# Performance work log

Hardware: AMD Instinct MI355X
Metric: run time of the kernel (lower is better)

Reference implementation:

```python
import jax, jax.numpy as jnp
import numpy as np

PROP_TIME = 8  # matches init kwarg prop_time


def setup_inputs() -> dict:
    key = jax.random.key(0)
    k1, k2, k3, k4, k5 = jax.random.split(key, 5)
    B, H, W = 8, 480, 640
    return {
        "guided1": jax.random.normal(k1, (B, 9, H, W), dtype=jnp.float32),
        "guided2": jax.random.normal(k2, (B, 9, H, W), dtype=jnp.float32),
        "guided3": jax.random.normal(k3, (B, 9, H, W), dtype=jnp.float32),
        "fuse": jax.random.uniform(k4, (B, 3, H, W), dtype=jnp.float32),
        "x": jax.random.normal(k5, (B, 1, H, W), dtype=jnp.float32),
    }


def _neighbors(x, d):
    """Gather the 3x3 dilated neighborhood of a [B,1,H,W] map -> [B,9,H,W].
    Equivalent to F.unfold(x, 3, dilation=d, padding=d) reshaped to spatial."""
    B, _, H, W = x.shape
    xp = jnp.pad(x[:, 0], ((0, 0), (d, d), (d, d)))  # B, H+2d, W+2d
    return jnp.stack(
        [xp[:, i * d:i * d + H, j * d:j * d + W] for i in range(3) for j in range(3)],
        axis=1,
    )


def reference(guided1, guided2, guided3, fuse, x):
    # per-pixel affinity kernels, normalized over the 9 taps
    k1 = jax.nn.softmax(guided1, axis=1)
    k2 = jax.nn.softmax(guided2, axis=1)
    k3 = jax.nn.softmax(guided3, axis=1)
    f1, f2, f3 = fuse[:, 0:1], fuse[:, 1:2], fuse[:, 2:3]
    for _ in range(PROP_TIME):
        o1 = jnp.sum(_neighbors(x, 1) * k1, axis=1, keepdims=True)  # B,1,H,W
        o2 = jnp.sum(_neighbors(x, 2) * k2, axis=1, keepdims=True)
        o3 = jnp.sum(_neighbors(x, 3) * k3, axis=1, keepdims=True)
        x = o1 * f1 + o2 * f2 + o3 * f3
    return x
```

## Files before the change

### kernel.cpp

```cpp
#include <hip/hip_runtime.h>

typedef __attribute__((ext_vector_type(4))) float    float4v;
typedef __attribute__((ext_vector_type(8))) _Float16 half8v;
typedef __attribute__((ext_vector_type(4))) _Float16 half4v;

constexpr int B_ = 8;
constexpr int H_ = 480;
constexpr int W_ = 640;
constexpr int HW = H_ * W_;
constexpr int N  = B_ * HW;
constexpr int WPP = 28;

__global__ __launch_bounds__(256) void wprep_kernel(
    const float* __restrict__ g1, const float* __restrict__ g2,
    const float* __restrict__ g3, const float* __restrict__ fuse,
    _Float16* __restrict__ w)
{
    const int p  = blockIdx.x * 256 + threadIdx.x;
    const int b  = p / HW;
    const int hw = p - b * HW;

    _Float16 wl[WPP];
    wl[27] = (_Float16)0.f;

    const float* gs[3] = {g1, g2, g3};
#pragma unroll
    for (int d = 0; d < 3; ++d) {
        const float* gb = gs[d] + (size_t)b * 9 * HW + hw;
        float e[9];
        float m = -1e30f;
#pragma unroll
        for (int c = 0; c < 9; ++c) {
            e[c] = gb[(size_t)c * HW];
            m = fmaxf(m, e[c]);
        }
        float s = 0.f;
#pragma unroll
        for (int c = 0; c < 9; ++c) {
            e[c] = __expf(e[c] - m);
            s += e[c];
        }
        const float f = fuse[((size_t)b * 3 + d) * HW + hw] / s;
#pragma unroll
        for (int c = 0; c < 9; ++c)
            wl[d * 9 + c] = (_Float16)(e[c] * f);
    }

    _Float16* wp = w + (size_t)p * WPP;
    *(half8v*)(wp + 0)  = *(half8v*)(wl + 0);
    *(half8v*)(wp + 8)  = *(half8v*)(wl + 8);
    *(half8v*)(wp + 16) = *(half8v*)(wl + 16);
    *(half4v*)(wp + 24) = *(half4v*)(wl + 24);
}

__global__ __launch_bounds__(256) void prop_kernel(
    const float* __restrict__ xin, const _Float16* __restrict__ w,
    float* __restrict__ xout)
{
    const int j  = blockIdx.x * 64 + (threadIdx.x & 63);
    const int i  = blockIdx.y * 4  + (threadIdx.x >> 6);
    const int b  = blockIdx.z;
    const int hw = i * W_ + j;
    const int p  = b * HW + hw;

    const _Float16* wp = w + (size_t)p * WPP;
    const half8v w0 = *(const half8v*)(wp + 0);
    const half8v w1 = *(const half8v*)(wp + 8);
    const half8v w2 = *(const half8v*)(wp + 16);
    const half4v w3 = *(const half4v*)(wp + 24);

    _Float16 wl[27];
#pragma unroll
    for (int k = 0; k < 8; ++k) { wl[k] = w0[k]; wl[8 + k] = w1[k]; wl[16 + k] = w2[k]; }
#pragma unroll
    for (int k = 0; k < 3; ++k) wl[24 + k] = w3[k];

    const float* xb = xin + (size_t)b * HW;
    float acc = 0.f;
#pragma unroll
    for (int d = 1; d <= 3; ++d) {
#pragma unroll
        for (int ki = 0; ki < 3; ++ki) {
            const int ii = i + (ki - 1) * d;
            const bool vi = (unsigned)ii < (unsigned)H_;
#pragma unroll
            for (int kj = 0; kj < 3; ++kj) {
                const int jj = j + (kj - 1) * d;
                float xv = 0.f;
                if (vi && (unsigned)jj < (unsigned)W_)
                    xv = xb[ii * W_ + jj];
                acc = fmaf(xv, (float)wl[(d - 1) * 9 + ki * 3 + kj], acc);
            }
        }
    }
    xout[p] = acc;
}

extern "C" void kernel_launch(void* const* d_in, const int* in_sizes, int n_in,
                              void* d_out, int out_size, void* d_ws, size_t ws_size,
                              hipStream_t stream)
{
    const float* g1   = (const float*)d_in[0];
    const float* g2   = (const float*)d_in[1];
    const float* g3   = (const float*)d_in[2];
    const float* fuse = (const float*)d_in[3];
    const float* x    = (const float*)d_in[4];
    float* out = (float*)d_out;

    char* ws = (char*)d_ws;
    _Float16* w = (_Float16*)ws;
    float* xa = (float*)(ws + (size_t)N * WPP * 2);
    float* xb = xa + N;

    wprep_kernel<<<N / 256, 256, 0, stream>>>(g1, g2, g3, fuse, w);

    const dim3 pgrid(W_ / 64, H_ / 4, B_);
    const float* src = x;
    float* bufs[2] = {xa, xb};
    for (int t = 0; t < 8; ++t) {
        float* dst = (t == 7) ? out : bufs[t & 1];
        prop_kernel<<<pgrid, 256, 0, stream>>>(src, w, dst);
        src = dst;
    }
}
```

Baseline: 301.8 us.

## Fuse two propagation steps per launch with shared-memory halo tiles

Replaces the per-step propagation kernel with one that does two propagation iterations per launch. Each block stages a 52x80 input tile with a 6-pixel halo in LDS. It computes the intermediate step over a 46x72 region, holding the fp16 weights for 4 pixels per thread in registers, then writes that result back to LDS and computes the final 40x64 outputs. This halves the number of launches and global passes over the weight and x buffers. The cost is recomputing the halo, roughly 29% extra work on the first step, plus a large 832-thread block with higher register pressure.

New measurement: 366.4 us. 21.4% more time.

```diff
diff --git a/kernel.cpp b/kernel.cpp
--- a/kernel.cpp
+++ b/kernel.cpp
@@ -11,6 +11,15 @@
 constexpr int N  = B_ * HW;
 constexpr int WPP = 28;
 
+constexpr int TI = 40;
+constexpr int TJ = 64;
+constexpr int LR = 52;
+constexpr int LC = 80;
+constexpr int QROWS = 46;
+constexpr int QCOLS = 18;
+constexpr int NOWN  = QROWS * QCOLS;
+constexpr int BLK   = 832;
+
 __global__ __launch_bounds__(256) void wprep_kernel(
     const float* __restrict__ g1, const float* __restrict__ g2,
     const float* __restrict__ g3, const float* __restrict__ fuse,
@@ -53,47 +62,136 @@
     *(half4v*)(wp + 24) = *(half4v*)(wl + 24);
 }
 
-__global__ __launch_bounds__(256) void prop_kernel(
+__device__ __forceinline__ float wsel(const half8v& a, const half8v& b,
+                                      const half8v& c, const half4v& d, int t)
+{
+    if (t < 8)  return (float)a[t];
+    if (t < 16) return (float)b[t - 8];
+    if (t < 24) return (float)c[t - 16];
+    return (float)d[t - 24];
+}
+
+__global__ __launch_bounds__(BLK) void prop2_kernel(
     const float* __restrict__ xin, const _Float16* __restrict__ w,
     float* __restrict__ xout)
 {
-    const int j  = blockIdx.x * 64 + (threadIdx.x & 63);
-    const int i  = blockIdx.y * 4  + (threadIdx.x >> 6);
-    const int b  = blockIdx.z;
-    const int hw = i * W_ + j;
-    const int p  = b * HW + hw;
-
-    const _Float16* wp = w + (size_t)p * WPP;
-    const half8v w0 = *(const half8v*)(wp + 0);
-    const half8v w1 = *(const half8v*)(wp + 8);
-    const half8v w2 = *(const half8v*)(wp + 16);
-    const half4v w3 = *(const half4v*)(wp + 24);
-
-    _Float16 wl[27];
-#pragma unroll
-    for (int k = 0; k < 8; ++k) { wl[k] = w0[k]; wl[8 + k] = w1[k]; wl[16 + k] = w2[k]; }
-#pragma unroll
-    for (int k = 0; k < 3; ++k) wl[24 + k] = w3[k];
-
+    __shared__ float xs[LR * LC];
+
+    const int tid   = threadIdx.x;
+    const int tileJ = blockIdx.x;
+    const int tileI = blockIdx.y;
+    const int b     = blockIdx.z;
+    const int ti0   = tileI * TI;
+    const int tj0   = tileJ * TJ;
     const float* xb = xin + (size_t)b * HW;
-    float acc = 0.f;
-#pragma unroll
-    for (int d = 1; d <= 3; ++d) {
-#pragma unroll
-        for (int ki = 0; ki < 3; ++ki) {
-            const int ii = i + (ki - 1) * d;
-            const bool vi = (unsigned)ii < (unsigned)H_;
-#pragma unroll
-            for (int kj = 0; kj < 3; ++kj) {
-                const int jj = j + (kj - 1) * d;
-                float xv = 0.f;
-                if (vi && (unsigned)jj < (unsigned)W_)
-                    xv = xb[ii * W_ + jj];
-                acc = fmaf(xv, (float)wl[(d - 1) * 9 + ki * 3 + kj], acc);
-            }
-        }
-    }
-    xout[p] = acc;
+
+    for (int idx = tid; idx < LR * LC / 4; idx += BLK) {
+        const int r   = idx / (LC / 4);
+        const int q   = idx % (LC / 4);
+        const int gi  = ti0 + r - 6;
+        const int gj0 = tj0 + q * 4 - 8;
+        float4v v = {0.f, 0.f, 0.f, 0.f};
+        if ((unsigned)gi < (unsigned)H_) {
+            if (gj0 >= 0 && gj0 + 3 < W_) {
+                v = *(const float4v*)(xb + (size_t)gi * W_ + gj0);
+            } else {
+#pragma unroll
+                for (int k = 0; k < 4; ++k) {
+                    const int gj = gj0 + k;
+                    if ((unsigned)gj < (unsigned)W_) v[k] = xb[(size_t)gi * W_ + gj];
+                }
+            }
+        }
+        *(float4v*)&xs[r * LC + q * 4] = v;
+    }
+
+    const bool owner = (tid < NOWN);
+    const int qr  = tid / QCOLS;
+    const int qc  = tid % QCOLS;
+    const int li  = 3 + qr;
+    const int lj0 = 4 + qc * 4;
+    const int gi  = ti0 + qr - 3;
+    const int gj0 = tj0 + qc * 4 - 4;
+
+    const half8v z8 = {0, 0, 0, 0, 0, 0, 0, 0};
+    const half4v z4 = {0, 0, 0, 0};
+    half8v w0[4] = {z8, z8, z8, z8};
+    half8v w1[4] = {z8, z8, z8, z8};
+    half8v w2[4] = {z8, z8, z8, z8};
+    half4v w3[4] = {z4, z4, z4, z4};
+
+    if (owner && (unsigned)gi < (unsigned)H_) {
+#pragma unroll
+        for (int k = 0; k < 4; ++k) {
+            const int gj = gj0 + k;
+            if ((unsigned)gj < (unsigned)W_) {
+                const _Float16* wp = w + ((size_t)b * HW + (size_t)gi * W_ + gj) * WPP;
+                w0[k] = *(const half8v*)(wp + 0);
+                w1[k] = *(const half8v*)(wp + 8);
+                w2[k] = *(const half8v*)(wp + 16);
+                w3[k] = *(const half4v*)(wp + 24);
+            }
+        }
+    }
+    __syncthreads();
+
+    float x1[4] = {0.f, 0.f, 0.f, 0.f};
+    if (owner) {
+#pragma unroll
+        for (int dd = 0; dd < 3; ++dd) {
+            const int d = dd + 1;
+#pragma unroll
+            for (int ki = 0; ki < 3; ++ki) {
+                const int base = (li + (ki - 1) * d) * LC + lj0;
+                float win[12];
+                *(float4v*)&win[0] = *(const float4v*)&xs[base - 4];
+                *(float4v*)&win[4] = *(const float4v*)&xs[base];
+                *(float4v*)&win[8] = *(const float4v*)&xs[base + 4];
+#pragma unroll
+                for (int kj = 0; kj < 3; ++kj) {
+                    const int t   = dd * 9 + ki * 3 + kj;
+                    const int off = (kj - 1) * d + 4;
+#pragma unroll
+                    for (int k = 0; k < 4; ++k)
+                        x1[k] = fmaf(win[off + k], wsel(w0[k], w1[k], w2[k], w3[k], t), x1[k]);
+                }
+            }
+        }
+    }
+    __syncthreads();
+
+    if (owner) {
+        float4v v; v[0] = x1[0]; v[1] = x1[1]; v[2] = x1[2]; v[3] = x1[3];
+        *(float4v*)&xs[li * LC + lj0] = v;
+    }
+    __syncthreads();
+
+    const bool outq = owner && (qr >= 3) && (qr < 3 + TI) && (qc >= 1) && (qc < 17);
+    if (outq) {
+        float x2[4] = {0.f, 0.f, 0.f, 0.f};
+#pragma unroll
+        for (int dd = 0; dd < 3; ++dd) {
+            const int d = dd + 1;
+#pragma unroll
+            for (int ki = 0; ki < 3; ++ki) {
+                const int base = (li + (ki - 1) * d) * LC + lj0;
+                float win[12];
+                *(float4v*)&win[0] = *(const float4v*)&xs[base - 4];
+                *(float4v*)&win[4] = *(const float4v*)&xs[base];
+                *(float4v*)&win[8] = *(const float4v*)&xs[base + 4];
+#pragma unroll
+                for (int kj = 0; kj < 3; ++kj) {
+                    const int t   = dd * 9 + ki * 3 + kj;
+                    const int off = (kj - 1) * d + 4;
+#pragma unroll
+                    for (int k = 0; k < 4; ++k)
+                        x2[k] = fmaf(win[off + k], wsel(w0[k], w1[k], w2[k], w3[k], t), x2[k]);
+                }
+            }
+        }
+        float4v v; v[0] = x2[0]; v[1] = x2[1]; v[2] = x2[2]; v[3] = x2[3];
+        *(float4v*)(xout + (size_t)b * HW + (size_t)gi * W_ + gj0) = v;
+    }
 }
 
 extern "C" void kernel_launch(void* const* d_in, const int* in_sizes, int n_in,
@@ -114,12 +212,9 @@
 
     wprep_kernel<<<N / 256, 256, 0, stream>>>(g1, g2, g3, fuse, w);
 
-    const dim3 pgrid(W_ / 64, H_ / 4, B_);
-    const float* src = x;
-    float* bufs[2] = {xa, xb};
-    for (int t = 0; t < 8; ++t) {
-        float* dst = (t == 7) ? out : bufs[t & 1];
-        prop_kernel<<<pgrid, 256, 0, stream>>>(src, w, dst);
-        src = dst;
-    }
-}
+    const dim3 pgrid(W_ / TJ, H_ / TI, B_);
+    prop2_kernel<<<pgrid, BLK, 0, stream>>>(x,  w, xa);
+    prop2_kernel<<<pgrid, BLK, 0, stream>>>(xa, w, xb);
+    prop2_kernel<<<pgrid, BLK, 0, stream>>>(xb, w, xa);
+    prop2_kernel<<<pgrid, BLK, 0, stream>>>(xa, w, out);
+}
```
